# Performance work log

Measured on AMD Instinct MI355X. Metric: run time of the kernel, lower is better.

The kernel has to match this reference:

```python
import jax, jax.numpy as jnp
import numpy as np

J = 7
Q = 12
T = 16000
STRIDE = 2 ** J            # subsample factor 128 -> 125 output samples
EPS_N = 1e-8
EPS_L = 1e-5
ALPHA = 0.7


def _filters():
    """Analytic Morlet-like filter bank in the Fourier domain (fixed constants)."""
    omega = np.arange(T, dtype=np.float64) / T          # normalized freq in [0,1)
    # first-order wavelets: Q per octave over J octaves -> J*Q filters
    xi1 = 0.5 * 2.0 ** (-(np.arange(J * Q) + 1.0) / Q)  # center freqs [P1]
    sig1 = xi1 * (2.0 ** (1.0 / Q) - 1.0) * 2.0
    psi1 = np.exp(-((omega[None, :] - xi1[:, None]) ** 2) / (2.0 * sig1[:, None] ** 2))
    # second-order wavelets: one per octave -> J filters
    xi2 = 0.5 * 2.0 ** (-(np.arange(J) + 1.0))
    sig2 = xi2 * 0.5
    psi2 = np.exp(-((omega[None, :] - xi2[:, None]) ** 2) / (2.0 * sig2[:, None] ** 2))
    # lowpass phi matched to 2^J subsampling; symmetric so lowpassed real stays real
    sig_phi = 0.4 / STRIDE
    phi = (np.exp(-(omega ** 2) / (2.0 * sig_phi ** 2))
           + np.exp(-((omega - 1.0) ** 2) / (2.0 * sig_phi ** 2)))
    # valid second-order paths: octave of psi2 strictly deeper than octave of psi1
    j1 = np.arange(J * Q) // Q                           # octave index of each psi1
    i1, i2 = np.nonzero(j1[:, None] < np.arange(J)[None, :])
    return (jnp.asarray(psi1, jnp.float32), jnp.asarray(psi2, jnp.float32),
            jnp.asarray(phi, jnp.float32), i1, i2)

PSI1, PSI2, PHI, I1, I2 = _filters()   # C = 1 + 84 + 252 = 337 channels


def setup_inputs() -> dict:
    key = jax.random.key(0)
    x = jax.random.normal(key, (8, T), dtype=jnp.float32)
    return {"x": x}


def _scatter(x):
    # Hann-based tapering window (0.92*hann + 0.08), periodic like torch.hann_window
    n = jnp.arange(T, dtype=x.dtype)
    window = 0.92 * (0.5 * (1.0 - jnp.cos(2.0 * jnp.pi * n / T))) + 0.08
    x = x * window[None, :]                                  # [B, T]
    X = jnp.fft.fft(x)                                       # [B, T] complex
    # order 0: lowpass + subsample
    S0 = jnp.fft.ifft(X * PHI).real[:, ::STRIDE][:, None, :]  # [B, 1, 125]
    # order 1: |x * psi1| then lowpass + subsample
    U1 = jnp.abs(jnp.fft.ifft(X[:, None, :] * PSI1[None, :, :]))  # [B, P1, T]
    U1h = jnp.fft.fft(U1)
    S1 = jnp.fft.ifft(U1h * PHI).real[:, :, ::STRIDE]             # [B, P1, 125]
    # order 2: ||x*psi1| * psi2| along valid (j1, j2) paths, then lowpass
    U2 = jnp.abs(jnp.fft.ifft(U1h[:, I1, :] * PSI2[I2][None, :, :]))  # [B, P, T]
    S2 = jnp.fft.ifft(jnp.fft.fft(U2) * PHI).real[:, :, ::STRIDE]     # [B, P, 125]
    return jnp.concatenate([S0, S1, S2], axis=1)                     # [B, 337, 125]


def reference(x):
    Sx = _scatter(x)
    # eval-mode normalization: channel_mean=0, channel_std=1 buffers
    Sx_n = Sx / (1.0 + EPS_N)
    sign = jnp.sign(Sx_n)
    log_t = sign * jnp.log1p(jnp.abs(Sx_n) / EPS_L) * EPS_L
    return ALPHA * Sx_n + (1.0 - ALPHA) * log_t
```

## Files before the change

### kernel.cpp

```cpp
#include <hip/hip_runtime.h>

#define TN 16000

constexpr int nrad(int L){
  return (L%10==0) ? 10 : (L%5==0) ? 5 : (L>=8 && L!=16) ? 8 : (L>=4) ? 4 : 2;
}

__device__ __forceinline__ float2 cmulf(float2 a, float2 b){
  return make_float2(a.x*b.x - a.y*b.y, a.x*b.y + a.y*b.x);
}
__device__ __forceinline__ float2 cadd(float2 a, float2 b){ return make_float2(a.x+b.x, a.y+b.y); }
__device__ __forceinline__ float2 csub(float2 a, float2 b){ return make_float2(a.x-b.x, a.y-b.y); }

template<int L>
__device__ __forceinline__ int f2p(int k){
  if constexpr (L == 1) return 0;
  else {
    constexpr int R = nrad(L);
    return (k % R) * (L / R) + f2p<L / R>(k / R);
  }
}
template<int L>
__device__ __forceinline__ int p2f(int p){
  if constexpr (L == 1) return 0;
  else {
    constexpr int R = nrad(L);
    const int hi = p / (L / R);
    const int lo = p - hi * (L / R);
    return hi + R * p2f<L / R>(lo);
  }
}

template<bool SWZ>
__device__ __forceinline__ int sx(int i){ return SWZ ? (i ^ ((i >> 7) & 7)) : i; }

template<bool INV>
__device__ __forceinline__ void dft5c(float2* t){
  const float CR[5]={1.f,0.30901699437494742f,-0.80901699437494745f,
                     -0.80901699437494745f,0.30901699437494742f};
  const float CI[5]={0.f,-0.95105651629515357f,-0.58778525229247313f,
                     0.58778525229247313f,0.95105651629515357f};
  float2 y[5];
#pragma unroll
  for (int i=0;i<5;i++) y[i]=t[i];
#pragma unroll
  for (int u=0;u<5;u++){
    float zr=0.f, zi=0.f;
#pragma unroll
    for (int k=0;k<5;k++){
      const int m=(k*u)%5;
      const float wr=CR[m];
      const float wi=INV? -CI[m]:CI[m];
      zr += y[k].x*wr - y[k].y*wi;
      zi += y[k].x*wi + y[k].y*wr;
    }
    t[u]=make_float2(zr,zi);
  }
}

template<bool INV>
__device__ __forceinline__ void dft4c(float2* a){
  float2 s02=cadd(a[0],a[2]), d02=csub(a[0],a[2]);
  float2 s13=cadd(a[1],a[3]), d13=csub(a[1],a[3]);
  a[0]=cadd(s02,s13); a[2]=csub(s02,s13);
  if constexpr (INV){
    a[1]=make_float2(d02.x-d13.y, d02.y+d13.x);
    a[3]=make_float2(d02.x+d13.y, d02.y-d13.x);
  } else {
    a[1]=make_float2(d02.x+d13.y, d02.y-d13.x);
    a[3]=make_float2(d02.x-d13.y, d02.y+d13.x);
  }
}

template<bool INV>
__device__ __forceinline__ void dft8(float2* y){
  float2 e[4]={y[0],y[2],y[4],y[6]};
  float2 o[4]={y[1],y[3],y[5],y[7]};
  dft4c<INV>(e); dft4c<INV>(o);
  const float C=0.70710678118654752f;
  const float2 w1 = INV ? make_float2(C,C)   : make_float2(C,-C);
  const float2 w2 = INV ? make_float2(0.f,1.f): make_float2(0.f,-1.f);
  const float2 w3 = INV ? make_float2(-C,C)  : make_float2(-C,-C);
  float2 t;
  t=o[0];            y[0]=cadd(e[0],t); y[4]=csub(e[0],t);
  t=cmulf(o[1],w1);  y[1]=cadd(e[1],t); y[5]=csub(e[1],t);
  t=cmulf(o[2],w2);  y[2]=cadd(e[2],t); y[6]=csub(e[2],t);
  t=cmulf(o[3],w3);  y[3]=cadd(e[3],t); y[7]=csub(e[3],t);
}

template<bool INV>
__device__ __forceinline__ void dft10(float2* y){
  float2 e[5]={y[0],y[2],y[4],y[6],y[8]};
  float2 o[5]={y[1],y[3],y[5],y[7],y[9]};
  dft5c<INV>(e); dft5c<INV>(o);
  const float CR[5]={1.f,0.80901699437494745f,0.30901699437494742f,
                     -0.30901699437494742f,-0.80901699437494745f};
  const float SI[5]={0.f,0.58778525229247313f,0.95105651629515357f,
                     0.95105651629515357f,0.58778525229247313f};
#pragma unroll
  for (int u=0;u<5;u++){
    const float2 w = make_float2(CR[u], INV ? SI[u] : -SI[u]);
    const float2 t = cmulf(o[u], w);
    y[u]   = cadd(e[u], t);
    y[u+5] = csub(e[u], t);
  }
}

template<bool INV>
__device__ __forceinline__ float2 w25c(int m){
  const float CR[17]={1.f,0.968583161f,0.876306680f,0.728968627f,0.535826795f,
                      0.309016994f,0.062790520f,-0.187381315f,-0.425779292f,
                      -0.637423990f,-0.809016994f,-0.929776486f,-0.992114701f,
                      -0.992114701f,-0.929776486f,-0.809016994f,-0.637423990f};
  const float SI[17]={0.f,0.248689887f,0.481753674f,0.684547106f,0.844327926f,
                      0.951056516f,0.998026728f,0.982287251f,0.904827052f,
                      0.770513243f,0.587785252f,0.368124553f,0.125333234f,
                      -0.125333234f,-0.368124553f,-0.587785252f,-0.770513243f};
  return make_float2(CR[m], INV ? SI[m] : -SI[m]);
}

template<bool INV>
__device__ __forceinline__ void dft25(float2* y){
  float2 g[25];
#pragma unroll
  for (int a=0;a<5;a++){
    float2 t[5];
#pragma unroll
    for (int b=0;b<5;b++) t[b]=y[a+5*b];
    dft5c<INV>(t);
#pragma unroll
    for (int c=0;c<5;c++){
      float2 v=t[c];
      const int m=a*c;
      if (m) v=cmulf(v, w25c<INV>(m));
      g[a+5*c]=v;
    }
  }
#pragma unroll
  for (int c=0;c<5;c++){
    float2 t[5];
#pragma unroll
    for (int a=0;a<5;a++) t[a]=g[a+5*c];
    dft5c<INV>(t);
#pragma unroll
    for (int d=0;d<5;d++) y[c+5*d]=t[d];
  }
}

template<int R, bool INV>
__device__ __forceinline__ void dftR(float2* y){
  if constexpr (R==2){ float2 a=y[0],b=y[1]; y[0]=cadd(a,b); y[1]=csub(a,b); }
  else if constexpr (R==4){ dft4c<INV>(y); }
  else if constexpr (R==5){ dft5c<INV>(y); }
  else if constexpr (R==8){ dft8<INV>(y); }
  else { dft10<INV>(y); }
}

template<int R, bool INV>
__device__ __forceinline__ void twiddles(float2* y, int j, float invL){
  if (j == 0) return;
  const float ang = (INV ? 6.28318530717958647692f : -6.28318530717958647692f)
                    * (float)j * invL;
  float s,c; __sincosf(ang,&s,&c);
  const float2 w = make_float2(c,s);
  float2 wp = w;
  y[1]=cmulf(y[1],wp);
#pragma unroll
  for (int u=2;u<R;u++){ wp=cmulf(wp,w); y[u]=cmulf(y[u],wp); }
}

template<bool INV>
__device__ __forceinline__ void twiddles25(float2* y, int j, float invL){
  if (j == 0) return;
  const float ang = (INV ? 6.28318530717958647692f : -6.28318530717958647692f)
                    * (float)j * invL;
  float s,c; __sincosf(ang,&s,&c);
  const float2 w1=make_float2(c,s);
  __sincosf(5.f*ang,&s,&c);
  const float2 w5=make_float2(c,s);
  float2 Wb[5], Wa[5];
  Wb[1]=w1; Wb[2]=cmulf(w1,w1); Wb[3]=cmulf(Wb[2],w1); Wb[4]=cmulf(Wb[2],Wb[2]);
  Wa[1]=w5; Wa[2]=cmulf(w5,w5); Wa[3]=cmulf(Wa[2],w5); Wa[4]=cmulf(Wa[2],Wa[2]);
#pragma unroll
  for (int a=0;a<5;a++)
#pragma unroll
    for (int b=0;b<5;b++){
      const int u=5*a+b;
      if (u==0) continue;
      float2 v=y[u];
      if (a) v=cmulf(v,Wa[a]);
      if (b) v=cmulf(v,Wb[b]);
      y[u]=v;
    }
}

template<int N, int L, int R, bool INV, int EPI, bool SWZ>
__device__ void stageg(float2* buf, int tid, int nt, float esc){
  constexpr int M = L/R;
  constexpr float invL = 1.f/(float)L;
  for (int f = tid; f < N/R; f += nt){
    const int blk = f / M;
    const int j = f - blk*M;
    const int base = blk*L + j;
    float2 y[R];
#pragma unroll
    for (int t=0;t<R;t++) y[t]=buf[sx<SWZ>(base + t*M)];
    if constexpr (INV){
      twiddles<R,true>(y,j,invL);
      dftR<R,true>(y);
    } else {
      dftR<R,false>(y);
      twiddles<R,false>(y,j,invL);
    }
#pragma unroll
    for (int u=0;u<R;u++){
      if constexpr (EPI==1)
        buf[sx<SWZ>(base+u*M)]=make_float2(sqrtf(y[u].x*y[u].x+y[u].y*y[u].y)*esc, 0.f);
      else
        buf[sx<SWZ>(base+u*M)]=y[u];
    }
  }
}

template<int N, int L, bool SWZ>
__device__ void fwd_rec(float2* buf, int tid, int nt){
  if constexpr (L > 1){
    constexpr int R = nrad(L);
    stageg<N,L,R,false,0,SWZ>(buf,tid,nt,0.f);
    __syncthreads();
    fwd_rec<N,L/R,SWZ>(buf,tid,nt);
  }
}
template<int N, int L, int EPI, bool SWZ>
__device__ void inv_rec(float2* buf, int tid, int nt, float esc){
  if constexpr (L > 1){
    constexpr int R = nrad(L);
    inv_rec<N,L/R,0,SWZ>(buf,tid,nt,0.f);
    stageg<N,L,R,true,(L==N?EPI:0),SWZ>(buf,tid,nt,esc);
    __syncthreads();
  }
}

__device__ __forceinline__ float norm_val(float s){
  const float lt = log1pf(fabsf(s)*1.0e5f)*1.0e-5f;
  return 0.7f*s + 0.3f*copysignf(lt, s);
}

__global__ __launch_bounds__(256) void k_split(const float* __restrict__ x,
                                               float2* __restrict__ Xmid,
                                               float* __restrict__ out){
  __shared__ float sseg[4384];
  __shared__ float stab[412];
  const int tid = threadIdx.x;
  if (blockIdx.x >= 20){
    const int s = blockIdx.x - 20;
    const int b = s >> 2;
    const int o0 = (s & 3) * 32;
    const float* xb = x + b*TN;
    const int n0 = o0*128 - 204;
    for (int i=tid;i<4377;i+=256){
      int n = n0 + i;
      n += (n < 0) ? TN : 0;
      n -= (n >= TN) ? TN : 0;
      const float c=__cosf((float)n*(6.28318530717958647692f/16000.0f));
      sseg[i]=xb[n]*(0.08f+0.46f*(1.0f-c));
    }
    for (int i=tid;i<409;i+=256){
      const float dd=(float)(i-204);
      stab[i]=0.0078332134f*__expf(-1.9276571e-4f*dd*dd);
    }
    __syncthreads();
    const int o=tid>>3, g=tid&7;
    float acc=0.f;
    for (int d=-204+g; d<=204; d+=8)
      acc += stab[d+204]*sseg[o*128 + 204 - d];
    acc += __shfl_xor(acc,1); acc += __shfl_xor(acc,2); acc += __shfl_xor(acc,4);
    if (g==0 && o0+o<125) out[(size_t)b*337*125 + o0+o]=norm_val(acc);
    return;
  }
  const int gid = blockIdx.x*256 + tid;
  const int b = gid/640, j = gid - (gid/640)*640;
  const float* xb = x + b*TN;
  float2 y[25];
#pragma unroll
  for (int t=0;t<25;t++){
    const int n=j+640*t;
    const float c=__cosf((float)n*(6.28318530717958647692f/16000.0f));
    y[t]=make_float2(xb[n]*(0.08f+0.46f*(1.0f-c)), 0.f);
  }
  dft25<false>(y);
  twiddles25<false>(y, j, 1.f/16000.f);
  float2* Xm = Xmid + (size_t)b*TN;
#pragma unroll
  for (int u=0;u<25;u++) Xm[u*640+j]=y[u];
}

__global__ __launch_bounds__(128) void k_sub(const float2* __restrict__ Xmid,
                                             float2* __restrict__ Xnat){
  __shared__ float2 sb[640];
  const int tid=threadIdx.x;
  const int b=blockIdx.x/25, u0=blockIdx.x%25;
  const float2* src = Xmid + (size_t)b*TN + u0*640;
  for (int i=tid;i<640;i+=128) sb[i]=src[i];
  __syncthreads();
  fwd_rec<640,640,false>(sb,tid,128);
  float2* Xb = Xnat + (size_t)b*TN;
  for (int m=tid;m<640;m+=128) Xb[u0+25*m]=sb[f2p<640>(m)];
}

template<int W, int NT>
__device__ void o1body(const float2* __restrict__ Xnat, float2* __restrict__ U1h,
                       float* __restrict__ out, int b, int p1, int tid,
                       float2* buf, float* htab, int store_n, int zero_to){
  constexpr float TAU = 16000.f/(float)W;
  constexpr int DMAX = (204*W + TN-1)/TN;
  constexpr int OSTEP = W/125;
  for (int i=tid; i<2*DMAX+1; i+=NT){
    const float dd = TAU*(float)(i-DMAX);
    htab[i]=0.0078332134f*__expf(-1.9276571e-4f*dd*dd);
  }
  const float xi = 0.5f*exp2f(-(float)(p1+1)*(1.0f/12.0f));
  const float sg = xi*0.11892618871859045f;
  const float niv = -1.f/(2.f*sg*sg);
  int k0 = (int)(16000.f*(xi+4.45f*sg)) + 1 - W;
  if (k0 < 0) k0 = 0;
  const float2* Xb = Xnat + (size_t)b*TN;
  for (int p=tid;p<W;p+=NT){
    const int k = k0 + p2f<W>(p);
    const float d=(float)k*(1.f/16000.f)-xi;
    const float g=__expf(niv*d*d);
    const float2 v=Xb[k];
    buf[sx<true>(p)]=make_float2(v.x*g, v.y*g);
  }
  __syncthreads();
  inv_rec<W,W,1,true>(buf,tid,NT,1.f/16000.f);
  constexpr int G = (NT >= 1024) ? 8 : (NT >= 512) ? 4 : 1;
  {
    const int o = (G>1) ? (tid/G) : tid;
    const int g = (G>1) ? (tid%G) : 0;
    float acc=0.f;
    if (o<125){
      for (int d=-DMAX+g; d<=DMAX; d+=G){
        int ix=o*OSTEP-d;
        ix += (ix<0)?W:0; ix -= (ix>=W)?W:0;
        acc += htab[d+DMAX]*buf[sx<true>(ix)].x;
      }
    }
    if constexpr (G==8){ acc += __shfl_xor(acc,1); acc += __shfl_xor(acc,2); acc += __shfl_xor(acc,4); }
    else if constexpr (G==4){ acc += __shfl_xor(acc,1); acc += __shfl_xor(acc,2); }
    if (o<125 && g==0) out[((size_t)b*337+1+p1)*125+o]=norm_val(TAU*acc);
  }
  if (store_n>0){
    __syncthreads();
    fwd_rec<W,W,true>(buf,tid,NT);
    float2* Ub = U1h + (size_t)(b*84+p1)*8000;
    for (int k=tid;k<store_n;k+=NT){
      const float2 v=buf[sx<true>(f2p<W>(k))];
      Ub[k]=make_float2(TAU*v.x, TAU*v.y);
    }
    for (int k=store_n+tid;k<zero_to;k+=NT) Ub[k]=make_float2(0.f,0.f);
  }
}

template<int W, int NT, int MP>
__device__ void o1body_mp(const float2* __restrict__ Xnat, float2* __restrict__ U1h,
                          float* __restrict__ out, int a, int r0, int tid,
                          float2* bufall, float* htab, int store_n, int zero_to){
  constexpr int PT = NT/MP;
  constexpr int WP = W+8;
  constexpr float TAU = 16000.f/(float)W;
  constexpr int DMAX = (204*W + TN-1)/TN;
  constexpr int OSTEP = W/125;
  for (int i=tid; i<2*DMAX+1; i+=NT){
    const float dd = TAU*(float)(i-DMAX);
    htab[i]=0.0078332134f*__expf(-1.9276571e-4f*dd*dd);
  }
  const int sub = tid/PT, lt = tid - sub*PT;
  const int r = r0 + sub;
  const int b = r/12, p1 = a*12 + (r%12);
  float2* buf = bufall + sub*WP;
  const float xi = 0.5f*exp2f(-(float)(p1+1)*(1.0f/12.0f));
  const float sg = xi*0.11892618871859045f;
  const float niv = -1.f/(2.f*sg*sg);
  int k0 = (int)(16000.f*(xi+4.45f*sg)) + 1 - W;
  if (k0 < 0) k0 = 0;
  const float2* Xb = Xnat + (size_t)b*TN;
  for (int p=lt;p<W;p+=PT){
    const int k = k0 + p2f<W>(p);
    const float d=(float)k*(1.f/16000.f)-xi;
    const float g=__expf(niv*d*d);
    const float2 v=Xb[k];
    buf[sx<true>(p)]=make_float2(v.x*g, v.y*g);
  }
  __syncthreads();
  inv_rec<W,W,1,true>(buf,lt,PT,1.f/16000.f);
  for (int o=lt;o<125;o+=PT){
    float acc=0.f;
    for (int d=-DMAX; d<=DMAX; ++d){
      int ix=o*OSTEP-d;
      ix += (ix<0)?W:0; ix -= (ix>=W)?W:0;
      acc += htab[d+DMAX]*buf[sx<true>(ix)].x;
    }
    out[((size_t)b*337+1+p1)*125+o]=norm_val(TAU*acc);
  }
  if (store_n>0){
    __syncthreads();
    fwd_rec<W,W,true>(buf,lt,PT);
    float2* Ub = U1h + (size_t)(b*84+p1)*8000;
    for (int k=lt;k<store_n;k+=PT){
      const float2 v=buf[sx<true>(f2p<W>(k))];
      Ub[k]=make_float2(TAU*v.x, TAU*v.y);
    }
    for (int k=store_n+lt;k<zero_to;k+=PT) Ub[k]=make_float2(0.f,0.f);
  }
}

__global__ __launch_bounds__(1024) void k_order1(const float2* __restrict__ Xnat,
                                                 float2* __restrict__ U1h,
                                                 float* __restrict__ out){
  __shared__ float2 buf[8064];
  __shared__ float htab[257];
  const int tid=threadIdx.x;
  const int id=blockIdx.x;
  if (id < 96){
    const int b=id/12, p1=id%12;
    o1body<8000,1024>(Xnat,U1h,out,b,p1,tid,buf,htab,8000,8000);
  } else if (id < 144){
    o1body_mp<4000,1024,2>(Xnat,U1h,out,1,(id-96)*2,tid,buf,htab,4000,4000);
  } else if (id < 168){
    o1body_mp<2000,1024,4>(Xnat,U1h,out,2,(id-144)*4,tid,buf,htab,2000,2000);
  } else if (id < 180){
    o1body_mp<1000,1024,8>(Xnat,U1h,out,3,(id-168)*8,tid,buf,htab,1000,1000);
  } else if (id < 192){
    o1body_mp< 625,1024,8>(Xnat,U1h,out,4,(id-180)*8,tid,buf,htab, 625,1000);
  } else if (id < 204){
    o1body_mp< 500,1024,8>(Xnat,U1h,out,5,(id-192)*8,tid,buf,htab, 500, 500);
  } else {
    o1body_mp< 250,1024,8>(Xnat,U1h,out,6,(id-204)*8,tid,buf,htab,   0,   0);
  }
}

template<int N, int NT>
__device__ void o2body(const float2* __restrict__ U1h, float* __restrict__ out,
                       int b, int p1, int j2, int q, int tid,
                       float2* buf, float* htab){
  constexpr int R = TN/N;
  constexpr int CMAX = (204*N + TN-1)/TN;
  constexpr int OSTEP = 128/R;
  for (int i=tid; i<2*CMAX+1; i+=NT){
    const float dd = (float)((i-CMAX)*R);
    htab[i]=0.0078332134f*__expf(-1.9276571e-4f*dd*dd);
  }
  const float xi = 0.5f*exp2f(-(float)(j2+1));
  const float sg = 0.5f*xi;
  const float niv = -1.f/(2.f*sg*sg);
  const float2* Zb = U1h + (size_t)(b*84+p1)*8000;
  for (int p=tid;p<N;p+=NT){
    const int k = p2f<N>(p);
    const float d=(float)k*(1.f/16000.f)-xi;
    const float g=__expf(niv*d*d);
    const float2 v=Zb[k];
    buf[sx<true>(p)]=make_float2(v.x*g, v.y*g);
  }
  __syncthreads();
  inv_rec<N,N,1,true>(buf,tid,NT,1.f/16000.f);
  constexpr int G = (NT >= 1024) ? 8 : (NT >= 512) ? 4 : 1;
  const int o = (G>1) ? (tid/G) : tid;
  const int g = (G>1) ? (tid%G) : 0;
  float acc=0.f;
  if (o<125){
    for (int c=-CMAX+g; c<=CMAX; c+=G){
      int ix=o*OSTEP-c;
      ix += (ix<0)?N:0; ix -= (ix>=N)?N:0;
      acc += htab[c+CMAX]*buf[sx<true>(ix)].x;
    }
  }
  if constexpr (G==8){ acc += __shfl_xor(acc,1); acc += __shfl_xor(acc,2); acc += __shfl_xor(acc,4); }
  else if constexpr (G==4){ acc += __shfl_xor(acc,1); acc += __shfl_xor(acc,2); }
  if (o<125 && g==0) out[((size_t)b*337+85+q)*125+o]=norm_val((float)R*acc);
}

template<int N, int NT, int MP>
__device__ void o2body_mp(const float2* __restrict__ U1h, float* __restrict__ out,
                          int j2, int id0, int tid, float2* bufall, float* htab){
  constexpr int PT = NT/MP;
  constexpr int NP = N+8;
  constexpr int R = TN/N;
  constexpr int CMAX = (204*N + TN-1)/TN;
  constexpr int OSTEP = 128/R;
  for (int i=tid; i<2*CMAX+1; i+=NT){
    const float dd = (float)((i-CMAX)*R);
    htab[i]=0.0078332134f*__expf(-1.9276571e-4f*dd*dd);
  }
  const int sub = tid/PT, lt = tid - sub*PT;
  const int npath=12*j2;
  const int id = id0 + sub;
  const int b=id/npath, p1=id%npath;
  const int a=p1/12, rr=p1%12;
  const int q=12*(6*a-(a*(a-1))/2)+rr*(6-a)+(j2-a-1);
  float2* buf = bufall + sub*NP;
  const float xi = 0.5f*exp2f(-(float)(j2+1));
  const float sg = 0.5f*xi;
  const float niv = -1.f/(2.f*sg*sg);
  const float2* Zb = U1h + (size_t)(b*84+p1)*8000;
  for (int p=lt;p<N;p+=PT){
    const int k = p2f<N>(p);
    const float d=(float)k*(1.f/16000.f)-xi;
    const float g=__expf(niv*d*d);
    const float2 v=Zb[k];
    buf[sx<true>(p)]=make_float2(v.x*g, v.y*g);
  }
  __syncthreads();
  inv_rec<N,N,1,true>(buf,lt,PT,1.f/16000.f);
  for (int o=lt;o<125;o+=PT){
    float acc=0.f;
    for (int c=-CMAX; c<=CMAX; ++c){
      int ix=o*OSTEP-c;
      ix += (ix<0)?N:0; ix -= (ix>=N)?N:0;
      acc += htab[c+CMAX]*buf[sx<true>(ix)].x;
    }
    out[((size_t)b*337+85+q)*125+o]=norm_val((float)R*acc);
  }
}

__global__ __launch_bounds__(1024) void k_order2(const float2* __restrict__ U1h,
                                                 float* __restrict__ out){
  __shared__ float2 buf[8064];
  __shared__ float htab[205];
  const int tid=threadIdx.x;
  const int id=blockIdx.x;
  if (id < 96){
    const int b=id/12, p1=id%12;
    const int q=6*p1;
    o2body<8000,1024>(U1h,out,b,p1,1,q,tid,buf,htab);
  } else if (id < 192){
    o2body_mp<4000,1024,2>(U1h,out,2,(id-96)*2,tid,buf,htab);
  } else if (id < 264){
    o2body_mp<2000,1024,4>(U1h,out,3,(id-192)*4,tid,buf,htab);
  } else if (id < 312){
    o2body_mp<1000,1024,8>(U1h,out,4,(id-264)*8,tid,buf,htab);
  } else if (id < 372){
    o2body_mp<1000,1024,8>(U1h,out,5,(id-312)*8,tid,buf,htab);
  } else {
    o2body_mp< 500,1024,8>(U1h,out,6,(id-372)*8,tid,buf,htab);
  }
}

extern "C" void kernel_launch(void* const* d_in, const int* in_sizes, int n_in,
                              void* d_out, int out_size, void* d_ws, size_t ws_size,
                              hipStream_t stream){
  (void)in_sizes; (void)n_in; (void)out_size; (void)ws_size;
  const float* x = (const float*)d_in[0];
  float* out = (float*)d_out;
  float2* Xmid = (float2*)d_ws;
  float2* Xnat = (float2*)((char*)d_ws + (size_t)8*TN*sizeof(float2));
  float2* U1h  = (float2*)((char*)d_ws + (size_t)16*TN*sizeof(float2));
  k_split <<<52,   256, 0, stream>>>(x, Xmid, out);
  k_sub   <<<200,  128, 0, stream>>>(Xmid, Xnat);
  k_order1<<<216, 1024, 0, stream>>>(Xnat, U1h, out);
  k_order2<<<444, 1024, 0, stream>>>(U1h, out);
}
```

Measured before the change: 95.85 us.

## Add radix-20 Cooley-Tukey FFT stages and halve block size with more blocks

Adds radix-20 (and radix-16) FFT stages built as an in-register two-level decomposition with constant inner twiddles, so the 8000-, 4000-, 2000- and 1000-point FFTs need fewer shared-memory passes and barriers. The order-1 and order-2 kernels also drop from 1024 to 512 threads per block, and the packing of small FFTs is reduced from 8 to 4 per block for several octaves, which raises the block count. Larger radices raise register pressure, and fewer threads per block means more loop iterations for each thread.

```diff
diff --git a/kernel.cpp b/kernel.cpp
--- a/kernel.cpp
+++ b/kernel.cpp
@@ -3,7 +3,8 @@
 #define TN 16000
 
 constexpr int nrad(int L){
-  return (L%10==0) ? 10 : (L%5==0) ? 5 : (L>=8 && L!=16) ? 8 : (L>=4) ? 4 : 2;
+  return (L%20==0) ? 20 : (L%10==0) ? 10 : (L%5==0) ? 5 :
+         (L>=8 && L!=16) ? 8 : (L>=4) ? 4 : 2;
 }
 
 __device__ __forceinline__ float2 cmulf(float2 a, float2 b){
@@ -106,47 +107,6 @@
   }
 }
 
-template<bool INV>
-__device__ __forceinline__ float2 w25c(int m){
-  const float CR[17]={1.f,0.968583161f,0.876306680f,0.728968627f,0.535826795f,
-                      0.309016994f,0.062790520f,-0.187381315f,-0.425779292f,
-                      -0.637423990f,-0.809016994f,-0.929776486f,-0.992114701f,
-                      -0.992114701f,-0.929776486f,-0.809016994f,-0.637423990f};
-  const float SI[17]={0.f,0.248689887f,0.481753674f,0.684547106f,0.844327926f,
-                      0.951056516f,0.998026728f,0.982287251f,0.904827052f,
-                      0.770513243f,0.587785252f,0.368124553f,0.125333234f,
-                      -0.125333234f,-0.368124553f,-0.587785252f,-0.770513243f};
-  return make_float2(CR[m], INV ? SI[m] : -SI[m]);
-}
-
-template<bool INV>
-__device__ __forceinline__ void dft25(float2* y){
-  float2 g[25];
-#pragma unroll
-  for (int a=0;a<5;a++){
-    float2 t[5];
-#pragma unroll
-    for (int b=0;b<5;b++) t[b]=y[a+5*b];
-    dft5c<INV>(t);
-#pragma unroll
-    for (int c=0;c<5;c++){
-      float2 v=t[c];
-      const int m=a*c;
-      if (m) v=cmulf(v, w25c<INV>(m));
-      g[a+5*c]=v;
-    }
-  }
-#pragma unroll
-  for (int c=0;c<5;c++){
-    float2 t[5];
-#pragma unroll
-    for (int a=0;a<5;a++) t[a]=g[a+5*c];
-    dft5c<INV>(t);
-#pragma unroll
-    for (int d=0;d<5;d++) y[c+5*d]=t[d];
-  }
-}
-
 template<int R, bool INV>
 __device__ __forceinline__ void dftR(float2* y){
   if constexpr (R==2){ float2 a=y[0],b=y[1]; y[0]=cadd(a,b); y[1]=csub(a,b); }
@@ -154,6 +114,63 @@
   else if constexpr (R==5){ dft5c<INV>(y); }
   else if constexpr (R==8){ dft8<INV>(y); }
   else { dft10<INV>(y); }
+}
+
+template<int NN, bool INV>
+__device__ __forceinline__ float2 wNc(int m){
+  if constexpr (NN==25){
+    const float CR[17]={1.f,0.968583161f,0.876306680f,0.728968627f,0.535826795f,
+                        0.309016994f,0.062790520f,-0.187381315f,-0.425779292f,
+                        -0.637423990f,-0.809016994f,-0.929776486f,-0.992114701f,
+                        -0.992114701f,-0.929776486f,-0.809016994f,-0.637423990f};
+    const float SI[17]={0.f,0.248689887f,0.481753674f,0.684547106f,0.844327926f,
+                        0.951056516f,0.998026728f,0.982287251f,0.904827052f,
+                        0.770513243f,0.587785252f,0.368124553f,0.125333234f,
+                        -0.125333234f,-0.368124553f,-0.587785252f,-0.770513243f};
+    return make_float2(CR[m], INV ? SI[m] : -SI[m]);
+  } else if constexpr (NN==20){
+    const float CR[13]={1.f,0.951056516f,0.809016994f,0.587785252f,0.309016994f,
+                        0.f,-0.309016994f,-0.587785252f,-0.809016994f,-0.951056516f,
+                        -1.f,-0.951056516f,-0.809016994f};
+    const float SI[13]={0.f,0.309016994f,0.587785252f,0.809016994f,0.951056516f,
+                        1.f,0.951056516f,0.809016994f,0.587785252f,0.309016994f,
+                        0.f,-0.309016994f,-0.587785252f};
+    return make_float2(CR[m], INV ? SI[m] : -SI[m]);
+  } else {
+    const float CR[10]={1.f,0.923879533f,0.707106781f,0.382683432f,0.f,
+                        -0.382683432f,-0.707106781f,-0.923879533f,-1.f,-0.923879533f};
+    const float SI[10]={0.f,0.382683432f,0.707106781f,0.923879533f,1.f,
+                        0.923879533f,0.707106781f,0.382683432f,0.f,-0.382683432f};
+    return make_float2(CR[m], INV ? SI[m] : -SI[m]);
+  }
+}
+
+template<bool INV>
+__device__ __forceinline__ void dft25(float2* y){
+  float2 g[25];
+#pragma unroll
+  for (int a=0;a<5;a++){
+    float2 t[5];
+#pragma unroll
+    for (int b=0;b<5;b++) t[b]=y[a+5*b];
+    dft5c<INV>(t);
+#pragma unroll
+    for (int c=0;c<5;c++){
+      float2 v=t[c];
+      const int m=a*c;
+      if (m) v=cmulf(v, wNc<25,INV>(m));
+      g[a+5*c]=v;
+    }
+  }
+#pragma unroll
+  for (int c=0;c<5;c++){
+    float2 t[5];
+#pragma unroll
+    for (int a=0;a<5;a++) t[a]=g[a+5*c];
+    dft5c<INV>(t);
+#pragma unroll
+    for (int d=0;d<5;d++) y[c+5*d]=t[d];
+  }
 }
 
 template<int R, bool INV>
@@ -222,11 +239,103 @@
   }
 }
 
+template<int N, int L, int R1, int R2, bool INV, int EPI, bool SWZ>
+__device__ void stageCT(float2* buf, int tid, int nt, float esc){
+  constexpr int R = R1*R2;
+  constexpr int M = L/R;
+  constexpr float invL = 1.f/(float)L;
+  for (int f = tid; f < N/R; f += nt){
+    const int blk = f / M;
+    const int j = f - blk*M;
+    const int base = blk*L + j;
+    float2 y[R];
+    if constexpr (INV){
+      const float ang = 6.28318530717958647692f*(float)j*invL;
+      float s,c; __sincosf(ang,&s,&c);
+      const float2 w1 = make_float2(c,s);
+      float2 pa[R1];
+      pa[0]=make_float2(1.f,0.f);
+#pragma unroll
+      for (int a=1;a<R1;a++) pa[a]=cmulf(pa[a-1],w1);
+      const float2 wR1 = cmulf(pa[R1-1], w1);
+      float2 wb = make_float2(1.f,0.f);
+#pragma unroll
+      for (int b=0;b<R2;b++){
+#pragma unroll
+        for (int a=0;a<R1;a++){
+          float2 v = buf[sx<SWZ>(base+(a+R1*b)*M)];
+          y[a+R1*b] = cmulf(v, cmulf(pa[a], wb));
+        }
+        wb = cmulf(wb, wR1);
+      }
+    } else {
+#pragma unroll
+      for (int i=0;i<R;i++) y[i]=buf[sx<SWZ>(base+i*M)];
+    }
+#pragma unroll
+    for (int a=0;a<R1;a++){
+      float2 t[R2];
+#pragma unroll
+      for (int b=0;b<R2;b++) t[b]=y[a+R1*b];
+      dftR<R2,INV>(t);
+#pragma unroll
+      for (int c=0;c<R2;c++){
+        float2 v=t[c];
+        if (a*c) v=cmulf(v, wNc<R,INV>(a*c));
+        y[a+R1*c]=v;
+      }
+    }
+    float2 w1 = make_float2(1.f,0.f);
+    float2 pd[R1];
+    if constexpr (!INV){
+      const float ang = -6.28318530717958647692f*(float)j*invL;
+      float s,c; __sincosf(ang,&s,&c);
+      w1 = make_float2(c,s);
+      float2 wr2 = w1;
+#pragma unroll
+      for (int q=1;q<R2;q++) wr2 = cmulf(wr2, w1);
+      pd[0]=make_float2(1.f,0.f);
+#pragma unroll
+      for (int d=1;d<R1;d++) pd[d]=cmulf(pd[d-1],wr2);
+    }
+    float2 wc = make_float2(1.f,0.f);
+#pragma unroll
+    for (int c=0;c<R2;c++){
+      float2 t[R1];
+#pragma unroll
+      for (int a=0;a<R1;a++) t[a]=y[a+R1*c];
+      dftR<R1,INV>(t);
+#pragma unroll
+      for (int d=0;d<R1;d++){
+        const int u=c+R2*d;
+        float2 v=t[d];
+        if constexpr (!INV) v = cmulf(v, cmulf(wc, pd[d]));
+        if constexpr (EPI==1)
+          buf[sx<SWZ>(base+u*M)]=make_float2(sqrtf(v.x*v.x+v.y*v.y)*esc, 0.f);
+        else
+          buf[sx<SWZ>(base+u*M)]=v;
+      }
+      if constexpr (!INV) wc = cmulf(wc, w1);
+    }
+  }
+}
+
+template<int N, int L, int R, bool INV, int EPI, bool SWZ>
+__device__ __forceinline__ void stage_any(float2* buf, int tid, int nt, float esc){
+  if constexpr (R >= 16){
+    constexpr int R1 = (R==16)?4:5;
+    constexpr int R2 = R/R1;
+    stageCT<N,L,R1,R2,INV,EPI,SWZ>(buf,tid,nt,esc);
+  } else {
+    stageg<N,L,R,INV,EPI,SWZ>(buf,tid,nt,esc);
+  }
+}
+
 template<int N, int L, bool SWZ>
 __device__ void fwd_rec(float2* buf, int tid, int nt){
   if constexpr (L > 1){
     constexpr int R = nrad(L);
-    stageg<N,L,R,false,0,SWZ>(buf,tid,nt,0.f);
+    stage_any<N,L,R,false,0,SWZ>(buf,tid,nt,0.f);
     __syncthreads();
     fwd_rec<N,L/R,SWZ>(buf,tid,nt);
   }
@@ -236,7 +345,7 @@
   if constexpr (L > 1){
     constexpr int R = nrad(L);
     inv_rec<N,L/R,0,SWZ>(buf,tid,nt,0.f);
-    stageg<N,L,R,true,(L==N?EPI:0),SWZ>(buf,tid,nt,esc);
+    stage_any<N,L,R,true,(L==N?EPI:0),SWZ>(buf,tid,nt,esc);
     __syncthreads();
   }
 }
@@ -415,28 +524,28 @@
   }
 }
 
-__global__ __launch_bounds__(1024) void k_order1(const float2* __restrict__ Xnat,
-                                                 float2* __restrict__ U1h,
-                                                 float* __restrict__ out){
+__global__ __launch_bounds__(512) void k_order1(const float2* __restrict__ Xnat,
+                                                float2* __restrict__ U1h,
+                                                float* __restrict__ out){
   __shared__ float2 buf[8064];
   __shared__ float htab[257];
   const int tid=threadIdx.x;
   const int id=blockIdx.x;
   if (id < 96){
     const int b=id/12, p1=id%12;
-    o1body<8000,1024>(Xnat,U1h,out,b,p1,tid,buf,htab,8000,8000);
+    o1body<8000,512>(Xnat,U1h,out,b,p1,tid,buf,htab,8000,8000);
   } else if (id < 144){
-    o1body_mp<4000,1024,2>(Xnat,U1h,out,1,(id-96)*2,tid,buf,htab,4000,4000);
+    o1body_mp<4000,512,2>(Xnat,U1h,out,1,(id-96)*2,tid,buf,htab,4000,4000);
   } else if (id < 168){
-    o1body_mp<2000,1024,4>(Xnat,U1h,out,2,(id-144)*4,tid,buf,htab,2000,2000);
-  } else if (id < 180){
-    o1body_mp<1000,1024,8>(Xnat,U1h,out,3,(id-168)*8,tid,buf,htab,1000,1000);
+    o1body_mp<2000,512,4>(Xnat,U1h,out,2,(id-144)*4,tid,buf,htab,2000,2000);
   } else if (id < 192){
-    o1body_mp< 625,1024,8>(Xnat,U1h,out,4,(id-180)*8,tid,buf,htab, 625,1000);
-  } else if (id < 204){
-    o1body_mp< 500,1024,8>(Xnat,U1h,out,5,(id-192)*8,tid,buf,htab, 500, 500);
+    o1body_mp<1000,512,4>(Xnat,U1h,out,3,(id-168)*4,tid,buf,htab,1000,1000);
+  } else if (id < 216){
+    o1body_mp< 625,512,4>(Xnat,U1h,out,4,(id-192)*4,tid,buf,htab, 625,1000);
+  } else if (id < 240){
+    o1body_mp< 500,512,4>(Xnat,U1h,out,5,(id-216)*4,tid,buf,htab, 500, 500);
   } else {
-    o1body_mp< 250,1024,8>(Xnat,U1h,out,6,(id-204)*8,tid,buf,htab,   0,   0);
+    o1body_mp< 250,512,8>(Xnat,U1h,out,6,(id-240)*8,tid,buf,htab,   0,   0);
   }
 }
 
@@ -523,8 +632,8 @@
   }
 }
 
-__global__ __launch_bounds__(1024) void k_order2(const float2* __restrict__ U1h,
-                                                 float* __restrict__ out){
+__global__ __launch_bounds__(512) void k_order2(const float2* __restrict__ U1h,
+                                                float* __restrict__ out){
   __shared__ float2 buf[8064];
   __shared__ float htab[205];
   const int tid=threadIdx.x;
@@ -532,17 +641,17 @@
   if (id < 96){
     const int b=id/12, p1=id%12;
     const int q=6*p1;
-    o2body<8000,1024>(U1h,out,b,p1,1,q,tid,buf,htab);
+    o2body<8000,512>(U1h,out,b,p1,1,q,tid,buf,htab);
   } else if (id < 192){
-    o2body_mp<4000,1024,2>(U1h,out,2,(id-96)*2,tid,buf,htab);
+    o2body_mp<4000,512,2>(U1h,out,2,(id-96)*2,tid,buf,htab);
   } else if (id < 264){
-    o2body_mp<2000,1024,4>(U1h,out,3,(id-192)*4,tid,buf,htab);
-  } else if (id < 312){
-    o2body_mp<1000,1024,8>(U1h,out,4,(id-264)*8,tid,buf,htab);
-  } else if (id < 372){
-    o2body_mp<1000,1024,8>(U1h,out,5,(id-312)*8,tid,buf,htab);
+    o2body_mp<2000,512,4>(U1h,out,3,(id-192)*4,tid,buf,htab);
+  } else if (id < 360){
+    o2body_mp<1000,512,4>(U1h,out,4,(id-264)*4,tid,buf,htab);
+  } else if (id < 480){
+    o2body_mp<1000,512,4>(U1h,out,5,(id-360)*4,tid,buf,htab);
   } else {
-    o2body_mp< 500,1024,8>(U1h,out,6,(id-372)*8,tid,buf,htab);
+    o2body_mp< 500,512,8>(U1h,out,6,(id-480)*8,tid,buf,htab);
   }
 }
 
@@ -555,8 +664,8 @@
   float2* Xmid = (float2*)d_ws;
   float2* Xnat = (float2*)((char*)d_ws + (size_t)8*TN*sizeof(float2));
   float2* U1h  = (float2*)((char*)d_ws + (size_t)16*TN*sizeof(float2));
-  k_split <<<52,   256, 0, stream>>>(x, Xmid, out);
-  k_sub   <<<200,  128, 0, stream>>>(Xmid, Xnat);
-  k_order1<<<216, 1024, 0, stream>>>(Xnat, U1h, out);
-  k_order2<<<444, 1024, 0, stream>>>(U1h, out);
-}
+  k_split <<<52,  256, 0, stream>>>(x, Xmid, out);
+  k_sub   <<<200, 128, 0, stream>>>(Xmid, Xnat);
+  k_order1<<<252, 512, 0, stream>>>(Xnat, U1h, out);
+  k_order2<<<552, 512, 0, stream>>>(U1h, out);
+}
```

Measured after the change: 96.30 us. Within noise of the previous version (+0.5%).
